# Kernel optimization log

Hardware: AMD Instinct MI355X
Metric: run time of the kernel (lower is better)

## Reference

```python
import jax, jax.numpy as jnp
import numpy as np

DIM = 1024
NUM_HEADS = 16
HEAD_DIM = DIM // NUM_HEADS
SCALE = HEAD_DIM ** -0.5
B, N = 4, 2048


def setup_inputs() -> dict:
    key = jax.random.key(0)
    ks = jax.random.split(key, 8)
    s = DIM ** -0.5
    x = jax.random.normal(ks[0], (B, N, DIM), dtype=jnp.float32)
    mask = jax.random.randint(ks[1], (B, N, N), 0, 2, dtype=jnp.int32)
    wq = jax.random.normal(ks[2], (DIM, DIM), dtype=jnp.float32) * s
    wk = jax.random.normal(ks[3], (DIM, DIM), dtype=jnp.float32) * s
    wv = jax.random.normal(ks[4], (DIM, DIM), dtype=jnp.float32) * s
    wp = jax.random.normal(ks[5], (DIM, DIM), dtype=jnp.float32) * s
    bp = jnp.zeros((DIM,), dtype=jnp.float32)
    return {"x": x, "mask": mask, "wq": wq, "wk": wk, "wv": wv, "wp": wp, "bp": bp}


def reference(x, mask, wq, wk, wv, wp, bp):
    Bn, Nn, C = x.shape
    # torch Linear: y = x @ W^T; split heads -> (B, H, N, hd)
    def split_heads(y):
        return y.reshape(Bn, Nn, NUM_HEADS, HEAD_DIM).transpose(0, 2, 1, 3)
    q = split_heads(x @ wq.T)
    k = split_heads(x @ wk.T)
    v = split_heads(x @ wv.T)
    attn = jnp.einsum('bhqd,bhkd->bhqk', q, k) * SCALE  # (B,H,N,N)
    # mask==0 -> -inf; mask is (B,N,N), broadcast over heads
    attn = jnp.where(mask[:, None, :, :] == 0, -jnp.inf, attn)
    attn = jax.nn.softmax(attn, axis=-1)
    out = jnp.einsum('bhqk,bhkd->bhqd', attn, v)  # (B,H,N,hd)
    out = out.transpose(0, 2, 1, 3).reshape(Bn, Nn, C)
    return out @ wp.T + bp
```

## Files before the change

kernel.cpp:

```cpp
#include <hip/hip_runtime.h>
#include <stdint.h>

#define DIM 1024
#define NH 16
#define HD 64
#define BB 4
#define SS 2048
#define MR (BB*SS)
#define QSCALE 0.125f
#define L2E 1.44269504f

typedef float f32x4 __attribute__((ext_vector_type(4)));
typedef float f32x16 __attribute__((ext_vector_type(16)));
typedef __bf16 bf16x8 __attribute__((ext_vector_type(8)));
typedef uint32_t u32x4 __attribute__((ext_vector_type(4)));

typedef __attribute__((address_space(3))) void lds_void;
typedef __attribute__((address_space(1))) void glob_void;
#define GLL16(gp, lp) __builtin_amdgcn_global_load_lds((glob_void*)(gp), (lds_void*)(lp), 16, 0, 0)

static __device__ __forceinline__ ushort f2bf(float f) {
  uint32_t u = __builtin_bit_cast(uint32_t, f);
  u += 0x7FFF + ((u >> 16) & 1);
  return (ushort)(u >> 16);
}

static __device__ __forceinline__ f32x16 mfma32(bf16x8 a, bf16x8 b, f32x16 c) {
  return __builtin_amdgcn_mfma_f32_32x32x16_bf16(a, b, c, 0, 0, 0);
}
static __device__ __forceinline__ uint32_t cvtpk(float lo, float hi) {
  uint32_t r;
  asm("v_cvt_pk_bf16_f32 %0, %1, %2" : "=v"(r) : "v"(lo), "v"(hi));
  return r;
}
static __device__ __forceinline__ void plswap(uint32_t &a, uint32_t &b) {
  asm("v_permlane32_swap_b32 %0, %1" : "+v"(a), "+v"(b));
}

__global__ void cvt_bf16(const float* __restrict__ in, ushort* __restrict__ out,
                         const int n4) {
  const int stride = gridDim.x * blockDim.x;
  for (int i = blockIdx.x * blockDim.x + threadIdx.x; i < n4; i += stride) {
    const float4 v = reinterpret_cast<const float4*>(in)[i];
    ushort4 o;
    o.x = f2bf(v.x); o.y = f2bf(v.y); o.z = f2bf(v.z); o.w = f2bf(v.w);
    reinterpret_cast<ushort4*>(out)[i] = o;
  }
}

__global__ void cvt_w4(const float* __restrict__ w0, const float* __restrict__ w1,
                       const float* __restrict__ w2, const float* __restrict__ w3,
                       ushort* __restrict__ out) {
  const int n4 = DIM * DIM;
  const int rsz = DIM * DIM / 4;
  const int stride = gridDim.x * blockDim.x;
  for (int i = blockIdx.x * blockDim.x + threadIdx.x; i < n4; i += stride) {
    const int r = i / rsz, j = i - r * rsz;
    const float* src = (r == 0) ? w0 : (r == 1) ? w1 : (r == 2) ? w2 : w3;
    const float sc = (r == 0) ? (QSCALE * L2E) : 1.0f;
    const float4 v = reinterpret_cast<const float4*>(src)[j];
    ushort4 o;
    o.x = f2bf(v.x * sc); o.y = f2bf(v.y * sc);
    o.z = f2bf(v.z * sc); o.w = f2bf(v.w * sc);
    reinterpret_cast<ushort4*>(out)[i] = o;
  }
}

__global__ void pack_mask(const int* __restrict__ m, uint32_t* __restrict__ bits,
                          const int npairs) {
  const int lane = threadIdx.x & 63;
  const int wid = (blockIdx.x * blockDim.x + threadIdx.x) >> 6;
  const int nw = (gridDim.x * blockDim.x) >> 6;
  for (int p = wid; p < npairs; p += nw) {
    const int v = m[(size_t)p * 64 + lane];
    const unsigned long long bal = __ballot(v != 0);
    if (lane == 0) reinterpret_cast<unsigned long long*>(bits)[p] = bal;
  }
}

template<int EPI>
__global__ __launch_bounds__(256)
void gemm128(const ushort* __restrict__ A, const ushort* __restrict__ Bm,
             const int N, const int K,
             ushort* __restrict__ q_out, ushort* __restrict__ k_out,
             ushort* __restrict__ vt_out,
             const float* __restrict__ bias, float* __restrict__ c_out) {
  __shared__ __align__(16) ushort As[128 * 64];
  __shared__ __align__(16) ushort Bs[128 * 64];
  const int tid = threadIdx.x;
  const int lane = tid & 63, w = tid >> 6;
  const int l31 = lane & 31, hi = lane >> 5;
  const int gx = gridDim.x;
  int lin = blockIdx.y * gx + blockIdx.x;
  const int qch = (gx * gridDim.y) >> 3;
  lin = (lin & 7) * qch + (lin >> 3);
  const int tm = (lin / gx) * 128;
  const int tn = (lin % gx) * 128;
  const int wm = (w >> 1) * 64;
  const int wn = (w & 1) * 64;

  f32x16 acc[2][2] = {};

  const int srow = w * 32 + (lane >> 3);
  const int scol = ((lane & 7) ^ (lane >> 3)) * 8;
  const ushort* aptr = A + (size_t)(tm + srow) * K + scol;
  const ushort* bptr = Bm + (size_t)(tn + srow) * K + scol;
  ushort* lA = As + (size_t)(w * 32) * 64;
  ushort* lB = Bs + (size_t)(w * 32) * 64;

  const int swr = l31 & 7;

  for (int k0 = 0; k0 < K; k0 += 64) {
#pragma unroll
    for (int it = 0; it < 4; ++it) {
      GLL16(aptr + k0 + (size_t)(it * 8) * K, lA + it * 8 * 64);
      GLL16(bptr + k0 + (size_t)(it * 8) * K, lB + it * 8 * 64);
    }
    __syncthreads();
    bf16x8 af[4][2], bfr[4][2];
#pragma unroll
    for (int kk = 0; kk < 4; ++kk) {
      const int slot = (2 * kk + hi) ^ swr;
#pragma unroll
      for (int t = 0; t < 2; ++t) {
        af[kk][t]  = *reinterpret_cast<const bf16x8*>(As + (wm + t * 32 + l31) * 64 + slot * 8);
        bfr[kk][t] = *reinterpret_cast<const bf16x8*>(Bs + (wn + t * 32 + l31) * 64 + slot * 8);
      }
    }
#pragma unroll
    for (int kk = 0; kk < 4; ++kk)
#pragma unroll
      for (int ti = 0; ti < 2; ++ti)
#pragma unroll
        for (int tj = 0; tj < 2; ++tj)
          acc[ti][tj] = mfma32(af[kk][ti], bfr[kk][tj], acc[ti][tj]);
    __syncthreads();
  }

#pragma unroll
  for (int ti = 0; ti < 2; ++ti) {
#pragma unroll
    for (int tj = 0; tj < 2; ++tj) {
      const int nc = tn + wn + tj * 32 + l31;
#pragma unroll
      for (int r = 0; r < 16; ++r) {
        const int mrow = tm + wm + ti * 32 + (r & 3) + 8 * (r >> 2) + 4 * hi;
        const float v = acc[ti][tj][r];
        if constexpr (EPI == 0) {
          const int bb = mrow >> 11, tok = mrow & (SS - 1);
          const int which = nc >> 10, cc = nc & (DIM - 1);
          const int h = cc >> 6, d = cc & 63;
          const size_t bh = (size_t)bb * NH + h;
          const ushort bv = f2bf(v);
          if (which == 0)      q_out[(bh * SS + tok) * HD + d] = bv;
          else if (which == 1) k_out[(bh * SS + tok) * HD + d] = bv;
          else                 vt_out[(bh * HD + d) * SS + tok] = bv;
        } else {
          c_out[(size_t)mrow * N + nc] = v + bias[nc];
        }
      }
    }
  }
}

__global__ __launch_bounds__(512)
void attn_kernel(const ushort* __restrict__ Q, const ushort* __restrict__ Kg,
                 const ushort* __restrict__ Vt, const uint32_t* __restrict__ mb,
                 ushort* __restrict__ O) {
  __shared__ __align__(16) ushort lds[16384];
  __shared__ float rl_lds[8][32];

  const int tid = threadIdx.x, lane = tid & 63, w = tid >> 6;
  const int l31 = lane & 31, hi = lane >> 5;
  const int d = blockIdx.x;
  const int g = d & 63, m = d >> 6;
  const int h = g & 15, b = g >> 4;
  const size_t bh = (size_t)b * NH + h;
  const int q0w = m * 256 + w * 32;
  const int qg = q0w + l31;

  bf16x8 qf[4];
  const ushort* qp = Q + (bh * SS + qg) * HD + hi * 8;
#pragma unroll
  for (int kk = 0; kk < 4; ++kk)
    qf[kk] = *reinterpret_cast<const bf16x8*>(qp + kk * 16);

  f32x16 oacc[2] = {};
  float lrun = 0.f;

  const ushort* kbase = Kg + bh * SS * HD;
  const ushort* vbase = Vt + bh * HD * SS;
  const uint32_t* mrow = mb + ((size_t)b * SS + qg) * (SS / 32);

  auto stage = [&](int buf, int kv0) {
    GLL16(kbase + (size_t)(kv0 + (w >> 2) * 32 + l31) * HD + (w & 3) * 16 + hi * 8,
          lds + buf * 8192 + w * 512);
    GLL16(vbase + (size_t)((w & 1) * 32 + l31) * SS + kv0 + (w >> 1) * 16 + hi * 8,
          lds + buf * 8192 + 4096 + w * 512);
  };

  stage(0, 0);
  uint2 mw = *reinterpret_cast<const uint2*>(mrow);
  int cur = 0;

  for (int kv0 = 0; kv0 < SS; kv0 += 64) {
    __syncthreads();
    uint2 mw_n = mw;
    if (kv0 + 64 < SS) {
      stage(cur ^ 1, kv0 + 64);
      mw_n = *reinterpret_cast<const uint2*>(mrow + ((kv0 + 64) >> 5));
    }

    const ushort* kf = lds + cur * 8192 + lane * 8;
    const ushort* vf = lds + cur * 8192 + 4096 + lane * 8;

    f32x16 st[2];
    __builtin_amdgcn_s_setprio(1);
#pragma unroll
    for (int t = 0; t < 2; ++t) {
      f32x16 s = {};
#pragma unroll
      for (int kk = 0; kk < 4; ++kk) {
        const bf16x8 kfrag = *reinterpret_cast<const bf16x8*>(kf + (t * 4 + kk) * 512);
        s = mfma32(kfrag, qf[kk], s);
      }
      st[t] = s;
    }
    __builtin_amdgcn_s_setprio(0);

    float p[2][16];
#pragma unroll
    for (int t = 0; t < 2; ++t) {
      const uint32_t wts = (t ? mw.y : mw.x) >> (4 * hi);
#pragma unroll
      for (int r = 0; r < 16; ++r) {
        const int sh = (r & 3) + 8 * (r >> 2);
        const float pe = __builtin_amdgcn_exp2f(((wts >> sh) & 1u) ? st[t][r] : -3e38f);
        p[t][r] = pe;
        lrun += pe;
      }
    }

    bf16x8 PA[4];
#pragma unroll
    for (int t = 0; t < 2; ++t) {
      uint32_t pk[8];
#pragma unroll
      for (int i = 0; i < 8; ++i)
        pk[i] = cvtpk(p[t][2 * i], p[t][2 * i + 1]);
      plswap(pk[0], pk[2]);
      plswap(pk[1], pk[3]);
      plswap(pk[4], pk[6]);
      plswap(pk[5], pk[7]);
      const u32x4 lo = {pk[0], pk[1], pk[2], pk[3]};
      const u32x4 hh = {pk[4], pk[5], pk[6], pk[7]};
      PA[2 * t]     = __builtin_bit_cast(bf16x8, lo);
      PA[2 * t + 1] = __builtin_bit_cast(bf16x8, hh);
    }

    __builtin_amdgcn_s_setprio(1);
#pragma unroll
    for (int c = 0; c < 4; ++c)
#pragma unroll
      for (int dt = 0; dt < 2; ++dt) {
        const bf16x8 vfrag = *reinterpret_cast<const bf16x8*>(vf + (c * 2 + dt) * 512);
        oacc[dt] = mfma32(PA[c], vfrag, oacc[dt]);
      }
    __builtin_amdgcn_s_setprio(0);

    mw = mw_n;
    cur ^= 1;
  }

  lrun += __shfl_xor(lrun, 32, 64);
  const float rl = 1.0f / lrun;
  if (lane < 32) rl_lds[w][lane] = rl;
  asm volatile("s_waitcnt lgkmcnt(0)" ::: "memory");
  f32x4 rg[4];
#pragma unroll
  for (int g2 = 0; g2 < 4; ++g2)
    rg[g2] = *reinterpret_cast<const f32x4*>(&rl_lds[w][g2 * 8 + 4 * hi]);
#pragma unroll
  for (int dt = 0; dt < 2; ++dt)
#pragma unroll
    for (int r = 0; r < 16; ++r) {
      const int qrow = q0w + (r & 3) + 8 * (r >> 2) + 4 * hi;
      const float v = oacc[dt][r] * rg[r >> 2][r & 3];
      O[((size_t)b * SS + qrow) * DIM + h * HD + dt * 32 + l31] = f2bf(v);
    }
}

extern "C" void kernel_launch(void* const* d_in, const int* in_sizes, int n_in,
                              void* d_out, int out_size, void* d_ws, size_t ws_size,
                              hipStream_t stream) {
  const float* x  = (const float*)d_in[0];
  const int* mask = (const int*)d_in[1];
  const float* wq = (const float*)d_in[2];
  const float* wk = (const float*)d_in[3];
  const float* wv = (const float*)d_in[4];
  const float* wp = (const float*)d_in[5];
  const float* bp = (const float*)d_in[6];
  float* out = (float*)d_out;

  ushort* xb   = (ushort*)d_ws;
  ushort* wcat = xb + (size_t)MR * DIM;
  ushort* wpb  = wcat + (size_t)3 * DIM * DIM;
  ushort* Qb   = wpb + (size_t)DIM * DIM;
  ushort* Kb   = Qb + (size_t)MR * DIM;
  ushort* Vtb  = Kb + (size_t)MR * DIM;
  ushort* Ob   = Vtb + (size_t)MR * DIM;
  uint32_t* mb = (uint32_t*)(Ob + (size_t)MR * DIM);
  const size_t needed = ((size_t)MR * DIM * 5 + (size_t)4 * DIM * DIM) * 2 + (size_t)BB * SS * (SS / 8);
  if (ws_size < needed) return;

  cvt_bf16<<<2048, 256, 0, stream>>>(x, xb, MR * DIM / 4);
  cvt_w4<<<2048, 256, 0, stream>>>(wq, wk, wv, wp, wcat);
  pack_mask<<<2048, 256, 0, stream>>>(mask, mb, BB * SS * SS / 64);

  gemm128<0><<<dim3(3 * DIM / 128, MR / 128), 256, 0, stream>>>(
      xb, wcat, 3 * DIM, DIM, Qb, Kb, Vtb, nullptr, nullptr);

  attn_kernel<<<512, 512, 0, stream>>>(Qb, Kb, Vtb, mb, Ob);

  gemm128<1><<<dim3(DIM / 128, MR / 128), 256, 0, stream>>>(
      Ob, wpb, DIM, DIM, nullptr, nullptr, nullptr, bp, out);
}
```

Before: 238.5 us.

## Pre-expand mask into per-lane bf16 AND masks and compute row sums via MFMA

Adds a mask packing kernel that expands the bit mask into 16-bit AND masks laid out to match the MFMA accumulator register order, so the attention inner loop applies the mask with a bitwise AND on packed bf16 probabilities instead of per-element shifts and selects. Row sums are now accumulated by an extra MFMA against a ones vector instead of scalar adds and a cross-lane shuffle/LDS reduction. The path runs only when the workspace is large enough for a 32 MiB expanded mask, which raises mask memory traffic per kv tile in exchange for fewer VALU ops. Row sums now come from bf16-rounded probabilities.

```diff
diff --git a/kernel.cpp b/kernel.cpp
--- a/kernel.cpp
+++ b/kernel.cpp
@@ -75,6 +75,46 @@
     const int v = m[(size_t)p * 64 + lane];
     const unsigned long long bal = __ballot(v != 0);
     if (lane == 0) reinterpret_cast<unsigned long long*>(bits)[p] = bal;
+  }
+}
+
+__global__ __launch_bounds__(256)
+void pack_mask_exp(const int* __restrict__ m, uint32_t* __restrict__ out) {
+  __shared__ uint32_t bits[64][2];
+  const int tid = threadIdx.x, lane = tid & 63, w = tid >> 6;
+  const int bid = blockIdx.x;
+  const int qb = bid & 31, chunk = (bid >> 5) & 31, b = bid >> 10;
+  const int q0 = qb * 64;
+  for (int qq = 0; qq < 16; ++qq) {
+    const int ql = w * 16 + qq;
+    const int v = m[((size_t)b * SS + q0 + ql) * SS + chunk * 64 + lane];
+    const unsigned long long bal = __ballot(v != 0);
+    if (lane == 0) {
+      bits[ql][0] = (uint32_t)bal;
+      bits[ql][1] = (uint32_t)(bal >> 32);
+    }
+  }
+  __syncthreads();
+  const int ql = tid & 63;
+  const int sh0tab[8] = {0, 2, 8, 10, 16, 18, 24, 26};
+#pragma unroll
+  for (int cc = 0; cc < 4; ++cc) {
+    const int c = (tid >> 6) * 4 + cc;
+    const int t = c >> 3, hi = (c >> 2) & 1, j = c & 3;
+    uint2 o;
+#pragma unroll
+    for (int w2 = 0; w2 < 2; ++w2) {
+      const int i = 2 * j + w2;
+      const int kvl = t * 32 + sh0tab[i] + 4 * hi;
+      const uint32_t wd = bits[ql][kvl >> 5];
+      const uint32_t b0 = (wd >> (kvl & 31)) & 1u;
+      const uint32_t b1 = (wd >> ((kvl & 31) + 1)) & 1u;
+      const uint32_t v = (b0 ? 0xFFFFu : 0u) | (b1 ? 0xFFFF0000u : 0u);
+      if (w2 == 0) o.x = v; else o.y = v;
+    }
+    const size_t idx =
+        ((((((size_t)b * 32 + chunk) * 2 + t) * 2 + hi) * 4 + j) * 2048) + q0 + ql;
+    reinterpret_cast<uint2*>(out)[idx] = o;
   }
 }
 
@@ -163,6 +203,7 @@
   }
 }
 
+template<bool EM>
 __global__ __launch_bounds__(512)
 void attn_kernel(const ushort* __restrict__ Q, const ushort* __restrict__ Kg,
                  const ushort* __restrict__ Vt, const uint32_t* __restrict__ mb,
@@ -185,12 +226,18 @@
   for (int kk = 0; kk < 4; ++kk)
     qf[kk] = *reinterpret_cast<const bf16x8*>(qp + kk * 16);
 
+  const u32x4 onesw = {0x3F803F80u, 0x3F803F80u, 0x3F803F80u, 0x3F803F80u};
+  const bf16x8 ones = __builtin_bit_cast(bf16x8, onesw);
+
   f32x16 oacc[2] = {};
+  f32x16 oacc2 = {};
   float lrun = 0.f;
 
   const ushort* kbase = Kg + bh * SS * HD;
   const ushort* vbase = Vt + bh * HD * SS;
-  const uint32_t* mrow = mb + ((size_t)b * SS + qg) * (SS / 32);
+  const uint32_t* mrow = EM
+      ? (mb + (size_t)b * 2097152 + hi * 16384 + (size_t)qg * 2)
+      : (mb + ((size_t)b * SS + qg) * (SS / 32));
 
   auto stage = [&](int buf, int kv0) {
     GLL16(kbase + (size_t)(kv0 + (w >> 2) * 32 + l31) * HD + (w & 3) * 16 + hi * 8,
@@ -200,16 +247,27 @@
   };
 
   stage(0, 0);
-  uint2 mw = *reinterpret_cast<const uint2*>(mrow);
+  uint2 mw;
+  if constexpr (!EM) mw = *reinterpret_cast<const uint2*>(mrow);
   int cur = 0;
 
   for (int kv0 = 0; kv0 < SS; kv0 += 64) {
     __syncthreads();
-    uint2 mw_n = mw;
-    if (kv0 + 64 < SS) {
-      stage(cur ^ 1, kv0 + 64);
-      mw_n = *reinterpret_cast<const uint2*>(mrow + ((kv0 + 64) >> 5));
-    }
+    uint2 mz[2][4];
+    uint2 mw_n;
+    if constexpr (EM) {
+      const uint32_t* mc = mrow + (size_t)(kv0 >> 6) * 65536;
+#pragma unroll
+      for (int t = 0; t < 2; ++t)
+#pragma unroll
+        for (int j = 0; j < 4; ++j)
+          mz[t][j] = *reinterpret_cast<const uint2*>(mc + t * 32768 + j * 4096);
+    } else {
+      mw_n = mw;
+      if (kv0 + 64 < SS)
+        mw_n = *reinterpret_cast<const uint2*>(mrow + ((kv0 + 64) >> 5));
+    }
+    if (kv0 + 64 < SS) stage(cur ^ 1, kv0 + 64);
 
     const ushort* kf = lds + cur * 8192 + lane * 8;
     const ushort* vf = lds + cur * 8192 + 4096 + lane * 8;
@@ -228,26 +286,31 @@
     }
     __builtin_amdgcn_s_setprio(0);
 
-    float p[2][16];
-#pragma unroll
-    for (int t = 0; t < 2; ++t) {
-      const uint32_t wts = (t ? mw.y : mw.x) >> (4 * hi);
-#pragma unroll
-      for (int r = 0; r < 16; ++r) {
-        const int sh = (r & 3) + 8 * (r >> 2);
-        const float pe = __builtin_amdgcn_exp2f(((wts >> sh) & 1u) ? st[t][r] : -3e38f);
-        p[t][r] = pe;
-        lrun += pe;
-      }
-    }
-
     bf16x8 PA[4];
 #pragma unroll
     for (int t = 0; t < 2; ++t) {
       uint32_t pk[8];
-#pragma unroll
-      for (int i = 0; i < 8; ++i)
-        pk[i] = cvtpk(p[t][2 * i], p[t][2 * i + 1]);
+      if constexpr (EM) {
+#pragma unroll
+        for (int i = 0; i < 8; ++i) {
+          pk[i] = cvtpk(__builtin_amdgcn_exp2f(st[t][2 * i]),
+                        __builtin_amdgcn_exp2f(st[t][2 * i + 1]));
+          pk[i] &= ((i & 1) ? mz[t][i >> 1].y : mz[t][i >> 1].x);
+        }
+      } else {
+        const uint32_t wts = (t ? mw.y : mw.x) >> (4 * hi);
+        float p[16];
+#pragma unroll
+        for (int r = 0; r < 16; ++r) {
+          const int sh = (r & 3) + 8 * (r >> 2);
+          const float pe = __builtin_amdgcn_exp2f(((wts >> sh) & 1u) ? st[t][r] : -3e38f);
+          p[r] = pe;
+          lrun += pe;
+        }
+#pragma unroll
+        for (int i = 0; i < 8; ++i)
+          pk[i] = cvtpk(p[2 * i], p[2 * i + 1]);
+      }
       plswap(pk[0], pk[2]);
       plswap(pk[1], pk[3]);
       plswap(pk[4], pk[6]);
@@ -260,34 +323,50 @@
 
     __builtin_amdgcn_s_setprio(1);
 #pragma unroll
-    for (int c = 0; c < 4; ++c)
+    for (int c = 0; c < 4; ++c) {
 #pragma unroll
       for (int dt = 0; dt < 2; ++dt) {
         const bf16x8 vfrag = *reinterpret_cast<const bf16x8*>(vf + (c * 2 + dt) * 512);
         oacc[dt] = mfma32(PA[c], vfrag, oacc[dt]);
       }
+      if constexpr (EM) oacc2 = mfma32(PA[c], ones, oacc2);
+    }
     __builtin_amdgcn_s_setprio(0);
 
-    mw = mw_n;
+    if constexpr (!EM) mw = mw_n;
     cur ^= 1;
   }
 
-  lrun += __shfl_xor(lrun, 32, 64);
-  const float rl = 1.0f / lrun;
-  if (lane < 32) rl_lds[w][lane] = rl;
-  asm volatile("s_waitcnt lgkmcnt(0)" ::: "memory");
-  f32x4 rg[4];
-#pragma unroll
-  for (int g2 = 0; g2 < 4; ++g2)
-    rg[g2] = *reinterpret_cast<const f32x4*>(&rl_lds[w][g2 * 8 + 4 * hi]);
-#pragma unroll
-  for (int dt = 0; dt < 2; ++dt)
-#pragma unroll
-    for (int r = 0; r < 16; ++r) {
-      const int qrow = q0w + (r & 3) + 8 * (r >> 2) + 4 * hi;
-      const float v = oacc[dt][r] * rg[r >> 2][r & 3];
-      O[((size_t)b * SS + qrow) * DIM + h * HD + dt * 32 + l31] = f2bf(v);
-    }
+  if constexpr (EM) {
+    float rls[16];
+#pragma unroll
+    for (int r = 0; r < 16; ++r) rls[r] = 1.0f / oacc2[r];
+#pragma unroll
+    for (int dt = 0; dt < 2; ++dt)
+#pragma unroll
+      for (int r = 0; r < 16; ++r) {
+        const int qrow = q0w + (r & 3) + 8 * (r >> 2) + 4 * hi;
+        const float v = oacc[dt][r] * rls[r];
+        O[((size_t)b * SS + qrow) * DIM + h * HD + dt * 32 + l31] = f2bf(v);
+      }
+  } else {
+    lrun += __shfl_xor(lrun, 32, 64);
+    const float rl = 1.0f / lrun;
+    if (lane < 32) rl_lds[w][lane] = rl;
+    asm volatile("s_waitcnt lgkmcnt(0)" ::: "memory");
+    f32x4 rg[4];
+#pragma unroll
+    for (int g2 = 0; g2 < 4; ++g2)
+      rg[g2] = *reinterpret_cast<const f32x4*>(&rl_lds[w][g2 * 8 + 4 * hi]);
+#pragma unroll
+    for (int dt = 0; dt < 2; ++dt)
+#pragma unroll
+      for (int r = 0; r < 16; ++r) {
+        const int qrow = q0w + (r & 3) + 8 * (r >> 2) + 4 * hi;
+        const float v = oacc[dt][r] * rg[r >> 2][r & 3];
+        O[((size_t)b * SS + qrow) * DIM + h * HD + dt * 32 + l31] = f2bf(v);
+      }
+  }
 }
 
 extern "C" void kernel_launch(void* const* d_in, const int* in_sizes, int n_in,
@@ -310,17 +389,22 @@
   ushort* Vtb  = Kb + (size_t)MR * DIM;
   ushort* Ob   = Vtb + (size_t)MR * DIM;
   uint32_t* mb = (uint32_t*)(Ob + (size_t)MR * DIM);
-  const size_t needed = ((size_t)MR * DIM * 5 + (size_t)4 * DIM * DIM) * 2 + (size_t)BB * SS * (SS / 8);
-  if (ws_size < needed) return;
+  const size_t base = ((size_t)MR * DIM * 5 + (size_t)4 * DIM * DIM) * 2;
+  const size_t needed_em = base + (size_t)8388608 * 4;
+  const size_t needed_sm = base + (size_t)BB * SS * (SS / 8);
+  const bool em = (ws_size >= needed_em);
+  if (!em && ws_size < needed_sm) return;
 
   cvt_bf16<<<2048, 256, 0, stream>>>(x, xb, MR * DIM / 4);
   cvt_w4<<<2048, 256, 0, stream>>>(wq, wk, wv, wp, wcat);
-  pack_mask<<<2048, 256, 0, stream>>>(mask, mb, BB * SS * SS / 64);
+  if (em) pack_mask_exp<<<4096, 256, 0, stream>>>(mask, mb);
+  else    pack_mask<<<2048, 256, 0, stream>>>(mask, mb, BB * SS * SS / 64);
 
   gemm128<0><<<dim3(3 * DIM / 128, MR / 128), 256, 0, stream>>>(
       xb, wcat, 3 * DIM, DIM, Qb, Kb, Vtb, nullptr, nullptr);
 
-  attn_kernel<<<512, 512, 0, stream>>>(Qb, Kb, Vtb, mb, Ob);
+  if (em) attn_kernel<true><<<512, 512, 0, stream>>>(Qb, Kb, Vtb, mb, Ob);
+  else    attn_kernel<false><<<512, 512, 0, stream>>>(Qb, Kb, Vtb, mb, Ob);
 
   gemm128<1><<<dim3(DIM / 128, MR / 128), 256, 0, stream>>>(
       Ob, wpb, DIM, DIM, nullptr, nullptr, nullptr, bp, out);
```

Result: slower. 258.7 us (+8.5%).
